# Optimization experiments

Hardware: AMD Instinct MI355X
Metric: run time of the kernel (lower is better)

## Reference

```python
import jax, jax.numpy as jnp
import numpy as np

N_USERS = 10000
N_ITEMS = 100000
N_FEATURES = 64
EMB_DIM = 128
TAU = 0.01
NUM_SEQ = 100000
SEQ_LEN = 50


def setup_inputs() -> dict:
    key = jax.random.key(0)
    k1, k2, k3, k4, k5, k6 = jax.random.split(key, 6)
    users = jax.random.randint(k1, (NUM_SEQ,), 0, N_USERS, dtype=jnp.int32)
    items = jax.random.randint(k2, (NUM_SEQ,), 0, N_ITEMS, dtype=jnp.int32)
    R_ui = jax.random.normal(k3, (NUM_SEQ, SEQ_LEN, N_FEATURES), dtype=jnp.float32)
    mask = jax.random.randint(k4, (NUM_SEQ, SEQ_LEN), 0, 2).astype(bool)
    mask = mask.at[:, 0].set(True)  # ensure every sequence has >=1 valid step
    w = jax.random.normal(k5, (N_FEATURES,), dtype=jnp.float32)  # nn.init.normal_
    item_emb = jax.random.normal(k6, (N_ITEMS + 1, EMB_DIM), dtype=jnp.float32) * 0.1
    item_emb = item_emb.at[0].set(0.0)  # padding_idx=0
    alpha = jnp.ones((1,), jnp.float32)
    beta = jnp.ones((1,), jnp.float32)
    gamma = jnp.ones((1,), jnp.float32)
    return {"users": users, "items": items, "R_ui": R_ui, "mask": mask,
            "w": w, "item_emb": item_emb, "alpha": alpha, "beta": beta, "gamma": gamma}


def reference(users, items, R_ui, mask, w, item_emb, alpha, beta, gamma):
    # Z: [num_seq, seq_len] masked power-mean features
    Z = jnp.einsum('nsd,d->ns', R_ui, w)
    Wv = jnp.maximum(Z, TAU)                       # nn.Threshold(tau, tau)
    Wp = jnp.where(mask, Wv ** alpha, 0.0)         # W[~mask] = 0, then **alpha
    W_alpha = jnp.sum(Wp, axis=-1) ** (1.0 / alpha)
    R_beta = jnp.sum(mask, axis=-1).astype(R_ui.dtype) ** beta
    wt = (W_alpha * R_beta) ** gamma               # [num_seq]
    q = item_emb[items]                            # [num_seq, emb_dim]
    # per-user weighted average (replaces Python loop over users.unique())
    num = jax.ops.segment_sum(wt[:, None] * q, users, num_segments=N_USERS + 1)
    den = jax.ops.segment_sum(wt, users, num_segments=N_USERS + 1)
    p = num[users] / den[users][:, None]
    r = jnp.sum(p * q, axis=-1)                    # [num_seq]
    return r
```

## Files before the change

kernel.cpp:

```cpp
#include <hip/hip_runtime.h>
#include <hip/hip_bf16.h>
#include <stdint.h>

#define N_USERS   10000
#define N_ITEMS   100000
#define N_FEAT    64
#define EMB_DIM   128
#define SEQ_LEN   50
#define TAU       0.01f

__global__ __launch_bounds__(256) void wt_kernel(
    const float* __restrict__ R, const void* __restrict__ mask_raw,
    const float* __restrict__ w,
    const float* __restrict__ alpha_p, const float* __restrict__ beta_p,
    const float* __restrict__ gamma_p,
    float* __restrict__ wt_out, int num_seq)
{
    int wave = (blockIdx.x * blockDim.x + threadIdx.x) >> 6;
    int lane = threadIdx.x & 63;
    if (wave >= num_seq) return;
    const int n = wave;

    const unsigned int* mi = (const unsigned int*)mask_raw;
    unsigned int pv = mi[lane];
    float        pf = __uint_as_float(pv);
    bool allint = __all(pv <= 1u) != 0;
    bool allflt = __all(pf == 0.0f || pf == 1.0f) != 0;
    const int mode = allint ? 0 : (allflt ? 1 : 2);

    bool mv = false;
    if (lane < SEQ_LEN) {
        size_t off = (size_t)n * SEQ_LEN + lane;
        if (mode == 0)      mv = ((const int*)mask_raw)[off] != 0;
        else if (mode == 1) mv = ((const float*)mask_raw)[off] != 0.0f;
        else                mv = ((const uint8_t*)mask_raw)[off] != 0;
    }
    unsigned long long mbits = __ballot(mv);

    const float alpha = alpha_p[0];
    const float beta  = beta_p[0];
    const float gamma = gamma_p[0];

    const int f4 = lane & 15;
    const int sg = lane >> 4;

    const float4 w4 = reinterpret_cast<const float4*>(w)[f4];
    const float4* Rn = reinterpret_cast<const float4*>(R + (size_t)n * SEQ_LEN * N_FEAT);

    float acc = 0.0f;
    float cnt = 0.0f;

    #pragma unroll
    for (int s0 = 0; s0 < SEQ_LEN; s0 += 4) {
        int s = s0 + sg;
        bool valid = (s < SEQ_LEN);
        float4 x = make_float4(0.f, 0.f, 0.f, 0.f);
        if (valid) x = Rn[s * (N_FEAT / 4) + f4];
        float d = x.x * w4.x + x.y * w4.y + x.z * w4.z + x.w * w4.w;
        d += __shfl_xor(d, 1);
        d += __shfl_xor(d, 2);
        d += __shfl_xor(d, 4);
        d += __shfl_xor(d, 8);
        if (valid && ((mbits >> s) & 1ULL)) {
            float Wv = fmaxf(d, TAU);
            acc += (alpha == 1.0f) ? Wv : powf(Wv, alpha);
            cnt += 1.0f;
        }
    }
    acc += __shfl_xor(acc, 16);
    acc += __shfl_xor(acc, 32);
    cnt += __shfl_xor(cnt, 16);
    cnt += __shfl_xor(cnt, 32);

    if (lane == 0) {
        float W_alpha = (alpha == 1.0f) ? acc : powf(acc, 1.0f / alpha);
        float R_beta  = (beta  == 1.0f) ? cnt : powf(cnt, beta);
        float base    = W_alpha * R_beta;
        wt_out[n]     = (gamma == 1.0f) ? base : powf(base, gamma);
    }
}

__global__ __launch_bounds__(256) void scatter_kernel(
    const int* __restrict__ users, const int* __restrict__ items,
    const float* __restrict__ wt, const float* __restrict__ item_emb,
    float* __restrict__ num, float* __restrict__ den, int num_seq)
{
    int idx = blockIdx.x * blockDim.x + threadIdx.x;
    int n = idx >> 7;
    int d = idx & 127;
    if (n >= num_seq) return;

    int u  = users[n];
    int it = items[n];
    float wtn = wt[n];
    float qd  = item_emb[(size_t)it * EMB_DIM + d];
    atomicAdd(&num[(size_t)u * EMB_DIM + d], wtn * qd);
    if (d == 0) atomicAdd(&den[u], wtn);
}

__global__ __launch_bounds__(256) void final_kernel(
    const int* __restrict__ users, const int* __restrict__ items,
    const float* __restrict__ item_emb,
    const float* __restrict__ num, const float* __restrict__ den,
    float* __restrict__ r, int num_seq)
{
    int wave = (blockIdx.x * blockDim.x + threadIdx.x) >> 6;
    int lane = threadIdx.x & 63;
    if (wave >= num_seq) return;
    const int n = wave;

    int u  = users[n];
    int it = items[n];
    float2 q = reinterpret_cast<const float2*>(item_emb + (size_t)it * EMB_DIM)[lane];
    float2 p = reinterpret_cast<const float2*>(num + (size_t)u * EMB_DIM)[lane];
    float dot = q.x * p.x + q.y * p.y;
    dot += __shfl_xor(dot, 1);
    dot += __shfl_xor(dot, 2);
    dot += __shfl_xor(dot, 4);
    dot += __shfl_xor(dot, 8);
    dot += __shfl_xor(dot, 16);
    dot += __shfl_xor(dot, 32);
    if (lane == 0) r[n] = dot / den[u];
}

extern "C" void kernel_launch(void* const* d_in, const int* in_sizes, int n_in,
                              void* d_out, int out_size, void* d_ws, size_t ws_size,
                              hipStream_t stream)
{
    const int*   users    = (const int*)d_in[0];
    const int*   items    = (const int*)d_in[1];
    const float* R_ui     = (const float*)d_in[2];
    const void*  mask     = d_in[3];
    const float* w        = (const float*)d_in[4];
    const float* item_emb = (const float*)d_in[5];
    const float* alpha    = (const float*)d_in[6];
    const float* beta     = (const float*)d_in[7];
    const float* gamma    = (const float*)d_in[8];

    const int num_seq = in_sizes[0];
    float* wt = (float*)d_out;
    float* num = (float*)d_ws;
    float* den = (float*)d_ws + (size_t)N_USERS * EMB_DIM;

    hipMemsetAsync(d_ws, 0, ((size_t)N_USERS * EMB_DIM + N_USERS) * sizeof(float),
                   stream);

    {
        int waves_per_block = 4;
        int blocks = (num_seq + waves_per_block - 1) / waves_per_block;
        wt_kernel<<<blocks, 256, 0, stream>>>(R_ui, mask, w, alpha, beta, gamma,
                                              wt, num_seq);
    }
    {
        long long threads = (long long)num_seq * EMB_DIM;
        int blocks = (int)((threads + 255) / 256);
        scatter_kernel<<<blocks, 256, 0, stream>>>(users, items, wt, item_emb,
                                                   num, den, num_seq);
    }
    {
        int waves_per_block = 4;
        int blocks = (num_seq + waves_per_block - 1) / waves_per_block;
        final_kernel<<<blocks, 256, 0, stream>>>(users, items, item_emb,
                                                 num, den, (float*)d_out, num_seq);
    }
}
```

Before: 303.9 us.

## Fuse weight computation with scatter-add and use nontemporal R loads

Merges the per-sequence weight kernel and the scatter kernel so each wave computes its weight and then atomically adds the weighted item embedding row into the user accumulator. This drops one launch and the write and re-read of the intermediate weight vector. R_ui is streamed with nontemporal loads so it pollutes the cache less. Each lane now issues two atomics instead of one thread per element, which changes atomic issue density.

After: 272.9 us. 10.2% less time.

```diff
diff --git a/kernel.cpp b/kernel.cpp
--- a/kernel.cpp
+++ b/kernel.cpp
@@ -9,17 +9,28 @@
 #define SEQ_LEN   50
 #define TAU       0.01f
 
-__global__ __launch_bounds__(256) void wt_kernel(
+typedef float f32x4 __attribute__((ext_vector_type(4)));
+
+__device__ inline f32x4 nt_load4(const float* p) {
+    return __builtin_nontemporal_load(reinterpret_cast<const f32x4*>(p));
+}
+
+__global__ __launch_bounds__(256) void wt_scatter_kernel(
     const float* __restrict__ R, const void* __restrict__ mask_raw,
     const float* __restrict__ w,
+    const int* __restrict__ users, const int* __restrict__ items,
+    const float* __restrict__ item_emb,
     const float* __restrict__ alpha_p, const float* __restrict__ beta_p,
     const float* __restrict__ gamma_p,
-    float* __restrict__ wt_out, int num_seq)
+    float* __restrict__ num, float* __restrict__ den, int num_seq)
 {
     int wave = (blockIdx.x * blockDim.x + threadIdx.x) >> 6;
     int lane = threadIdx.x & 63;
     if (wave >= num_seq) return;
     const int n = wave;
+
+    const int u  = users[n];
+    const int it = items[n];
 
     const unsigned int* mi = (const unsigned int*)mask_raw;
     unsigned int pv = mi[lane];
@@ -44,8 +55,8 @@
     const int f4 = lane & 15;
     const int sg = lane >> 4;
 
-    const float4 w4 = reinterpret_cast<const float4*>(w)[f4];
-    const float4* Rn = reinterpret_cast<const float4*>(R + (size_t)n * SEQ_LEN * N_FEAT);
+    const f32x4 w4 = *reinterpret_cast<const f32x4*>(w + 4 * f4);
+    const float* Rn = R + (size_t)n * SEQ_LEN * N_FEAT;
 
     float acc = 0.0f;
     float cnt = 0.0f;
@@ -54,8 +65,8 @@
     for (int s0 = 0; s0 < SEQ_LEN; s0 += 4) {
         int s = s0 + sg;
         bool valid = (s < SEQ_LEN);
-        float4 x = make_float4(0.f, 0.f, 0.f, 0.f);
-        if (valid) x = Rn[s * (N_FEAT / 4) + f4];
+        f32x4 x = {0.f, 0.f, 0.f, 0.f};
+        if (valid) x = nt_load4(Rn + s * N_FEAT + 4 * f4);
         float d = x.x * w4.x + x.y * w4.y + x.z * w4.z + x.w * w4.w;
         d += __shfl_xor(d, 1);
         d += __shfl_xor(d, 2);
@@ -72,30 +83,16 @@
     cnt += __shfl_xor(cnt, 16);
     cnt += __shfl_xor(cnt, 32);
 
-    if (lane == 0) {
-        float W_alpha = (alpha == 1.0f) ? acc : powf(acc, 1.0f / alpha);
-        float R_beta  = (beta  == 1.0f) ? cnt : powf(cnt, beta);
-        float base    = W_alpha * R_beta;
-        wt_out[n]     = (gamma == 1.0f) ? base : powf(base, gamma);
-    }
-}
+    float W_alpha = (alpha == 1.0f) ? acc : powf(acc, 1.0f / alpha);
+    float R_beta  = (beta  == 1.0f) ? cnt : powf(cnt, beta);
+    float base    = W_alpha * R_beta;
+    float wt      = (gamma == 1.0f) ? base : powf(base, gamma);
 
-__global__ __launch_bounds__(256) void scatter_kernel(
-    const int* __restrict__ users, const int* __restrict__ items,
-    const float* __restrict__ wt, const float* __restrict__ item_emb,
-    float* __restrict__ num, float* __restrict__ den, int num_seq)
-{
-    int idx = blockIdx.x * blockDim.x + threadIdx.x;
-    int n = idx >> 7;
-    int d = idx & 127;
-    if (n >= num_seq) return;
-
-    int u  = users[n];
-    int it = items[n];
-    float wtn = wt[n];
-    float qd  = item_emb[(size_t)it * EMB_DIM + d];
-    atomicAdd(&num[(size_t)u * EMB_DIM + d], wtn * qd);
-    if (d == 0) atomicAdd(&den[u], wtn);
+    const float2 q = reinterpret_cast<const float2*>(item_emb + (size_t)it * EMB_DIM)[lane];
+    float* numrow = num + (size_t)u * EMB_DIM;
+    atomicAdd(&numrow[2 * lane],     wt * q.x);
+    atomicAdd(&numrow[2 * lane + 1], wt * q.y);
+    if (lane == 0) atomicAdd(&den[u], wt);
 }
 
 __global__ __launch_bounds__(256) void final_kernel(
@@ -138,24 +135,19 @@
     const float* gamma    = (const float*)d_in[8];
 
     const int num_seq = in_sizes[0];
-    float* wt = (float*)d_out;
     float* num = (float*)d_ws;
     float* den = (float*)d_ws + (size_t)N_USERS * EMB_DIM;
 
-    hipMemsetAsync(d_ws, 0, ((size_t)N_USERS * EMB_DIM + N_USERS) * sizeof(float),
-                   stream);
+    (void)hipMemsetAsync(d_ws, 0,
+                         ((size_t)N_USERS * EMB_DIM + N_USERS) * sizeof(float),
+                         stream);
 
     {
         int waves_per_block = 4;
         int blocks = (num_seq + waves_per_block - 1) / waves_per_block;
-        wt_kernel<<<blocks, 256, 0, stream>>>(R_ui, mask, w, alpha, beta, gamma,
-                                              wt, num_seq);
-    }
-    {
-        long long threads = (long long)num_seq * EMB_DIM;
-        int blocks = (int)((threads + 255) / 256);
-        scatter_kernel<<<blocks, 256, 0, stream>>>(users, items, wt, item_emb,
-                                                   num, den, num_seq);
+        wt_scatter_kernel<<<blocks, 256, 0, stream>>>(R_ui, mask, w, users, items,
+                                                      item_emb, alpha, beta, gamma,
+                                                      num, den, num_seq);
     }
     {
         int waves_per_block = 4;
```
